# Kernel optimization log

Measured on AMD Instinct MI355X. Metric: run time of the kernel, lower is better.

Reference implementation:

```python
import jax, jax.numpy as jnp
import numpy as np

N = 50000      # nodes
E = 400000     # edges (before self loops)
IN = 128       # in_feat
HID = 64       # n_hidden per head
HEADS = [4, 4, 1]
NEG_SLOPE = 0.2  # DGL GATConv default


def gat_layer(h, src, dst, W, al, ar, b, n_nodes):
    # h: [N, Din]; W: [Din, H*F]; al/ar: [H, F]; b: [H*F]
    H, F = al.shape
    feat = (h @ W).reshape(n_nodes, H, F)              # [N,H,F]
    el = jnp.sum(feat * al, axis=-1)                   # [N,H]
    er = jnp.sum(feat * ar, axis=-1)                   # [N,H]
    e = jax.nn.leaky_relu(el[src] + er[dst], NEG_SLOPE)  # [E,H]
    # edge softmax over destination node segments (stable)
    e_max = jax.lax.stop_gradient(jax.ops.segment_max(e, dst, num_segments=n_nodes))
    ex = jnp.exp(e - e_max[dst])                       # [E,H]
    denom = jax.ops.segment_sum(ex, dst, num_segments=n_nodes)  # [N,H]
    alpha = ex / denom[dst]                            # [E,H]
    msg = feat[src] * alpha[:, :, None]                # [E,H,F]
    out = jax.ops.segment_sum(msg, dst, num_segments=n_nodes)   # [N,H,F]
    out = out + b.reshape(1, H, F)
    return out.reshape(n_nodes, H * F)


def setup_inputs() -> dict:
    key = jax.random.key(0)
    ks = jax.random.split(key, 16)
    inp = {
        "node_feat": jax.random.normal(ks[0], (N, IN), jnp.float32),
        "src": jax.random.randint(ks[1], (E,), 0, N),
        "dst": jax.random.randint(ks[2], (E,), 0, N),
    }
    dins = [IN, HID * HEADS[0], HID * HEADS[1]]
    for i, (din, h) in enumerate(zip(dins, HEADS)):
        k = 3 + 3 * i
        inp[f"W{i}"] = jax.random.normal(ks[k], (din, h * HID), jnp.float32) * 0.1
        inp[f"al{i}"] = jax.random.normal(ks[k + 1], (h, HID), jnp.float32) * 0.1
        inp[f"ar{i}"] = jax.random.normal(ks[k + 2], (h, HID), jnp.float32) * 0.1
        inp[f"b{i}"] = jnp.zeros((h * HID,), jnp.float32)
    return inp


def reference(node_feat, src, dst, W0, al0, ar0, b0, W1, al1, ar1, b1, W2, al2, ar2, b2):
    n_nodes = node_feat.shape[0]
    # add_self_loop
    loop = jnp.arange(n_nodes, dtype=src.dtype)
    src_a = jnp.concatenate([src, loop])
    dst_a = jnp.concatenate([dst, loop])
    h = node_feat
    h = gat_layer(h, src_a, dst_a, W0, al0, ar0, b0, n_nodes)  # [N, 4*64]
    h = gat_layer(h, src_a, dst_a, W1, al1, ar1, b1, n_nodes)  # [N, 4*64]
    h = gat_layer(h, src_a, dst_a, W2, al2, ar2, b2, n_nodes)  # [N, 64]
    return h
```

## Files before the change

kernel.cpp:

```cpp
#include <hip/hip_runtime.h>


typedef __attribute__((ext_vector_type(8))) short short8;
typedef __attribute__((ext_vector_type(4))) float f32x4;

__device__ __forceinline__ float bf2f(ushort u) {
  union { unsigned int i; float f; } c;
  c.i = ((unsigned int)u) << 16;
  return c.f;
}
__device__ __forceinline__ ushort f2bf(float f) {
  union { float f; unsigned int i; } c;
  c.f = f;
  unsigned int u = c.i;
  u += 0x7FFFu + ((u >> 16) & 1u);
  return (ushort)(u >> 16);
}
__device__ __forceinline__ float lrelu_exp(float x) {
  const float y = (x > 0.f) ? x : 0.2f * x;
  return __expf(y);
}

__global__ void convert_w_kernel(const float* __restrict__ W,
                                 ushort* __restrict__ Wt, int K, int N) {
  const int i = blockIdx.x * 256 + threadIdx.x;
  if (i >= K * N) return;
  const int k = i / N, n = i - k * N;
  Wt[n * K + k] = f2bf(W[i]);
}

template <bool AF32>
__global__ __launch_bounds__(256) void gemm_bf16_kernel(
    const void* __restrict__ Ap, const ushort* __restrict__ Wt,
    ushort* __restrict__ C, int M, int K, int Nc) {
  __shared__ ushort As[128][40];
  __shared__ ushort Bs[64][40];
  const int bm = blockIdx.x * 128;
  const int bn = blockIdx.y * 64;
  const int tid = threadIdx.x;
  const int lane = tid & 63;
  const int wave = tid >> 6;
  const int wm = wave >> 1;
  const int wn = wave & 1;
  const int ar = tid >> 1;
  const int ac = (tid & 1) * 16;
  const int brow = tid >> 2;
  const int bk = (tid & 3) * 8;
  const bool a_ok = (bm + ar) < M;

  f32x4 acc[4][2];
#pragma unroll
  for (int m = 0; m < 4; ++m)
#pragma unroll
    for (int n = 0; n < 2; ++n) acc[m][n] = 0.f;

  for (int k0 = 0; k0 < K; k0 += 32) {
    short8 h0, h1;
    if (AF32) {
      const float* A = (const float*)Ap;
      float buf[16];
      if (a_ok) {
        const float* p = A + (size_t)(bm + ar) * K + k0 + ac;
#pragma unroll
        for (int q = 0; q < 4; ++q) {
          float4 v = *(const float4*)(p + q * 4);
          buf[q * 4 + 0] = v.x;
          buf[q * 4 + 1] = v.y;
          buf[q * 4 + 2] = v.z;
          buf[q * 4 + 3] = v.w;
        }
      } else {
#pragma unroll
        for (int q = 0; q < 16; ++q) buf[q] = 0.f;
      }
#pragma unroll
      for (int q = 0; q < 8; ++q) h0[q] = (short)f2bf(buf[q]);
#pragma unroll
      for (int q = 0; q < 8; ++q) h1[q] = (short)f2bf(buf[8 + q]);
    } else {
      const ushort* A = (const ushort*)Ap;
      if (a_ok) {
        const ushort* p = A + (size_t)(bm + ar) * K + k0 + ac;
        h0 = *(const short8*)p;
        h1 = *(const short8*)(p + 8);
      } else {
        h0 = 0;
        h1 = 0;
      }
    }
    *(short8*)&As[ar][ac] = h0;
    *(short8*)&As[ar][ac + 8] = h1;
    *(short8*)&Bs[brow][bk] =
        *(const short8*)(Wt + (size_t)(bn + brow) * K + k0 + bk);
    __syncthreads();

    short8 a[4], b[2];
#pragma unroll
    for (int m = 0; m < 4; ++m)
      a[m] = *(const short8*)&As[wm * 64 + m * 16 + (lane & 15)][(lane >> 4) * 8];
#pragma unroll
    for (int n = 0; n < 2; ++n)
      b[n] = *(const short8*)&Bs[wn * 32 + n * 16 + (lane & 15)][(lane >> 4) * 8];
#pragma unroll
    for (int m = 0; m < 4; ++m)
#pragma unroll
      for (int n = 0; n < 2; ++n)
        acc[m][n] = __builtin_amdgcn_mfma_f32_16x16x32_bf16(a[m], b[n],
                                                            acc[m][n], 0, 0, 0);
    __syncthreads();
  }

#pragma unroll
  for (int m = 0; m < 4; ++m) {
#pragma unroll
    for (int r = 0; r < 4; ++r) {
      const int row = bm + wm * 64 + m * 16 + (lane >> 4) * 4 + r;
      if (row < M) {
#pragma unroll
        for (int n = 0; n < 2; ++n) {
          const int col = bn + wn * 32 + n * 16 + (lane & 15);
          C[(size_t)row * Nc + col] = f2bf(acc[m][n][r]);
        }
      }
    }
  }
}

__global__ __launch_bounds__(256) void attn_coef_h4(
    const ushort* __restrict__ feat, const float* __restrict__ al,
    const float* __restrict__ ar, float* __restrict__ el,
    float* __restrict__ er, int Nn) {
  const int n = (blockIdx.x * 256 + threadIdx.x) >> 6;
  const int lane = threadIdx.x & 63;
  if (n >= Nn) return;
  const short4 v = ((const short4*)(feat + (size_t)n * 256))[lane];
  const float4 a = ((const float4*)al)[lane];
  const float4 r = ((const float4*)ar)[lane];
  const float f0 = bf2f((ushort)v.x), f1 = bf2f((ushort)v.y),
              f2 = bf2f((ushort)v.z), f3 = bf2f((ushort)v.w);
  float pl = f0 * a.x + f1 * a.y + f2 * a.z + f3 * a.w;
  float pr = f0 * r.x + f1 * r.y + f2 * r.z + f3 * r.w;
#pragma unroll
  for (int off = 1; off < 16; off <<= 1) {
    pl += __shfl_xor(pl, off);
    pr += __shfl_xor(pr, off);
  }
  if ((lane & 15) == 0) {
    el[n * 4 + (lane >> 4)] = pl;
    er[n * 4 + (lane >> 4)] = pr;
  }
}

__global__ __launch_bounds__(256) void attn_coef_h1(
    const ushort* __restrict__ feat, const float* __restrict__ al,
    const float* __restrict__ ar, float* __restrict__ el,
    float* __restrict__ er, int Nn) {
  const int wid = (blockIdx.x * 256 + threadIdx.x) >> 6;
  const int lane = threadIdx.x & 63;
  const int n = wid * 4 + (lane >> 4);
  const int sub = lane & 15;
  if (n >= Nn) return;
  const short4 v = ((const short4*)(feat + (size_t)n * 64))[sub];
  const float4 a = ((const float4*)al)[sub];
  const float4 r = ((const float4*)ar)[sub];
  const float f0 = bf2f((ushort)v.x), f1 = bf2f((ushort)v.y),
              f2 = bf2f((ushort)v.z), f3 = bf2f((ushort)v.w);
  float pl = f0 * a.x + f1 * a.y + f2 * a.z + f3 * a.w;
  float pr = f0 * r.x + f1 * r.y + f2 * r.z + f3 * r.w;
#pragma unroll
  for (int off = 1; off < 16; off <<= 1) {
    pl += __shfl_xor(pl, off);
    pr += __shfl_xor(pr, off);
  }
  if (sub == 0) {
    el[n] = pl;
    er[n] = pr;
  }
}

__global__ void hist_kernel(const int* __restrict__ dst, int* __restrict__ cnt,
                            int E, int Nn) {
  const int e = blockIdx.x * blockDim.x + threadIdx.x;
  if (e >= E + Nn) return;
  const int d = (e < E) ? dst[e] : (e - E);
  atomicAdd(&cnt[d], 1);
}

__device__ __forceinline__ int block_incl_scan_1024(int x, int* lds16) {
  const int lane = threadIdx.x & 63;
  const int wid = threadIdx.x >> 6;
  int inc = x;
#pragma unroll
  for (int off = 1; off < 64; off <<= 1) {
    const int y = __shfl_up(inc, off);
    if (lane >= off) inc += y;
  }
  if (lane == 63) lds16[wid] = inc;
  __syncthreads();
  if (wid == 0) {
    int t = (lane < 16) ? lds16[lane] : 0;
#pragma unroll
    for (int off = 1; off < 16; off <<= 1) {
      const int y = __shfl_up(t, off);
      if (lane >= off) t += y;
    }
    if (lane < 16) lds16[lane] = t;
  }
  __syncthreads();
  if (wid > 0) inc += lds16[wid - 1];
  return inc;
}

__global__ __launch_bounds__(1024) void scan_blocks_kernel(
    const int* __restrict__ cnt, int* __restrict__ row_ptr,
    int* __restrict__ partials, int n) {
  __shared__ int lds16[16];
  const int i = blockIdx.x * 1024 + threadIdx.x;
  const int x = (i < n) ? cnt[i] : 0;
  const int inc = block_incl_scan_1024(x, lds16);
  if (i < n) row_ptr[i] = inc - x;
  if (threadIdx.x == 1023) partials[blockIdx.x] = inc;
}

__global__ __launch_bounds__(1024) void scan_partials_kernel(
    int* __restrict__ partials, int* __restrict__ row_ptr, int nb, int n) {
  __shared__ int lds16[16];
  const int x = (threadIdx.x < nb) ? partials[threadIdx.x] : 0;
  const int inc = block_incl_scan_1024(x, lds16);
  if (threadIdx.x < nb) partials[threadIdx.x] = inc - x;
  if (threadIdx.x == nb - 1) row_ptr[n] = inc;
}

__global__ __launch_bounds__(1024) void add_offsets_kernel(
    int* __restrict__ row_ptr, int* __restrict__ cursor,
    const int* __restrict__ partials, int n) {
  const int i = blockIdx.x * 1024 + threadIdx.x;
  if (i < n) {
    const int v = row_ptr[i] + partials[blockIdx.x];
    row_ptr[i] = v;
    cursor[i] = v;
  }
}

__global__ void scatter_kernel(const int* __restrict__ src,
                               const int* __restrict__ dst,
                               int* __restrict__ cursor, int* __restrict__ esrc,
                               int E, int Nn) {
  const int e = blockIdx.x * blockDim.x + threadIdx.x;
  if (e >= E + Nn) return;
  const int s = (e < E) ? src[e] : (e - E);
  const int d = (e < E) ? dst[e] : (e - E);
  const int pos = atomicAdd(&cursor[d], 1);
  esrc[pos] = s;
}

__global__ __launch_bounds__(256) void agg_fused_h4(
    const int* __restrict__ row_ptr, const int* __restrict__ esrc,
    const float* __restrict__ el, const float* __restrict__ er,
    const ushort* __restrict__ feat, const float* __restrict__ b,
    ushort* __restrict__ out, int Nn) {
  const int n = (blockIdx.x * 256 + threadIdx.x) >> 6;
  const int lane = threadIdx.x & 63;
  if (n >= Nn) return;
  const int h = lane >> 4;
  const int start = row_ptr[n];
  const int end = row_ptr[n + 1];
  const float erv = er[n * 4 + h];
  const short4* feat4 = (const short4*)feat;

  float den = 0.f;
  f32x4 acc = 0.f;
  int i = start;
  for (; i + 3 < end; i += 4) {
    const int s0 = esrc[i], s1 = esrc[i + 1], s2 = esrc[i + 2],
              s3 = esrc[i + 3];
    const float x0 = el[s0 * 4 + h] + erv;
    const float x1 = el[s1 * 4 + h] + erv;
    const float x2 = el[s2 * 4 + h] + erv;
    const float x3 = el[s3 * 4 + h] + erv;
    const short4 f0 = feat4[(size_t)s0 * 64 + lane];
    const short4 f1 = feat4[(size_t)s1 * 64 + lane];
    const short4 f2 = feat4[(size_t)s2 * 64 + lane];
    const short4 f3 = feat4[(size_t)s3 * 64 + lane];
    const float e0 = lrelu_exp(x0), e1 = lrelu_exp(x1), e2 = lrelu_exp(x2),
                e3 = lrelu_exp(x3);
    den += (e0 + e1) + (e2 + e3);
    acc[0] += e0 * bf2f((ushort)f0.x) + e1 * bf2f((ushort)f1.x) +
              e2 * bf2f((ushort)f2.x) + e3 * bf2f((ushort)f3.x);
    acc[1] += e0 * bf2f((ushort)f0.y) + e1 * bf2f((ushort)f1.y) +
              e2 * bf2f((ushort)f2.y) + e3 * bf2f((ushort)f3.y);
    acc[2] += e0 * bf2f((ushort)f0.z) + e1 * bf2f((ushort)f1.z) +
              e2 * bf2f((ushort)f2.z) + e3 * bf2f((ushort)f3.z);
    acc[3] += e0 * bf2f((ushort)f0.w) + e1 * bf2f((ushort)f1.w) +
              e2 * bf2f((ushort)f2.w) + e3 * bf2f((ushort)f3.w);
  }
  for (; i < end; ++i) {
    const int s = esrc[i];
    const float ex = lrelu_exp(el[s * 4 + h] + erv);
    const short4 f = feat4[(size_t)s * 64 + lane];
    den += ex;
    acc[0] += ex * bf2f((ushort)f.x);
    acc[1] += ex * bf2f((ushort)f.y);
    acc[2] += ex * bf2f((ushort)f.z);
    acc[3] += ex * bf2f((ushort)f.w);
  }
  const float rden = 1.f / den;
  const float4 bb = ((const float4*)b)[lane];
  short4 o;
  o.x = (short)f2bf(acc[0] * rden + bb.x);
  o.y = (short)f2bf(acc[1] * rden + bb.y);
  o.z = (short)f2bf(acc[2] * rden + bb.z);
  o.w = (short)f2bf(acc[3] * rden + bb.w);
  ((short4*)out)[(size_t)n * 64 + lane] = o;
}

__global__ __launch_bounds__(256) void agg_fused_h1(
    const int* __restrict__ row_ptr, const int* __restrict__ esrc,
    const float* __restrict__ el, const float* __restrict__ er,
    const ushort* __restrict__ feat, const float* __restrict__ b,
    float* __restrict__ out, int Nn) {
  const int n = (blockIdx.x * 256 + threadIdx.x) >> 6;
  const int lane = threadIdx.x & 63;
  if (n >= Nn) return;
  const int start = row_ptr[n];
  const int end = row_ptr[n + 1];
  const float erv = er[n];

  float den = 0.f;
  float acc = 0.f;
  int i = start;
  for (; i + 3 < end; i += 4) {
    const int s0 = esrc[i], s1 = esrc[i + 1], s2 = esrc[i + 2],
              s3 = esrc[i + 3];
    const float x0 = el[s0] + erv, x1 = el[s1] + erv, x2 = el[s2] + erv,
                x3 = el[s3] + erv;
    const ushort f0 = feat[(size_t)s0 * 64 + lane];
    const ushort f1 = feat[(size_t)s1 * 64 + lane];
    const ushort f2 = feat[(size_t)s2 * 64 + lane];
    const ushort f3 = feat[(size_t)s3 * 64 + lane];
    const float e0 = lrelu_exp(x0), e1 = lrelu_exp(x1), e2 = lrelu_exp(x2),
                e3 = lrelu_exp(x3);
    den += (e0 + e1) + (e2 + e3);
    acc += e0 * bf2f(f0) + e1 * bf2f(f1) + e2 * bf2f(f2) + e3 * bf2f(f3);
  }
  for (; i < end; ++i) {
    const int s = esrc[i];
    const float ex = lrelu_exp(el[s] + erv);
    den += ex;
    acc += ex * bf2f(feat[(size_t)s * 64 + lane]);
  }
  out[(size_t)n * 64 + lane] = acc * (1.f / den) + b[lane];
}

static void run_layer(const void* hin, bool af32, int K, int H, const float* W,
                      const float* al, const float* ar, const float* b,
                      ushort* Wt, ushort* feat, void* out, float* el,
                      float* er, const int* row_ptr, const int* esrc, int Nn,
                      hipStream_t stream) {
  const int HF = H * 64;
  convert_w_kernel<<<(K * HF + 255) / 256, 256, 0, stream>>>(W, Wt, K, HF);
  dim3 gg((Nn + 127) / 128, HF / 64);
  if (af32)
    gemm_bf16_kernel<true><<<gg, 256, 0, stream>>>(hin, Wt, feat, Nn, K, HF);
  else
    gemm_bf16_kernel<false><<<gg, 256, 0, stream>>>(hin, Wt, feat, Nn, K, HF);
  const int waves_grid = (Nn * 64 + 255) / 256;
  if (H == 4) {
    attn_coef_h4<<<waves_grid, 256, 0, stream>>>(feat, al, ar, el, er, Nn);
    agg_fused_h4<<<waves_grid, 256, 0, stream>>>(row_ptr, esrc, el, er, feat,
                                                 b, (ushort*)out, Nn);
  } else {
    attn_coef_h1<<<(Nn * 16 + 255) / 256, 256, 0, stream>>>(feat, al, ar, el,
                                                            er, Nn);
    agg_fused_h1<<<waves_grid, 256, 0, stream>>>(row_ptr, esrc, el, er, feat,
                                                 b, (float*)out, Nn);
  }
}

extern "C" void kernel_launch(void* const* d_in, const int* in_sizes, int n_in,
                              void* d_out, int out_size, void* d_ws,
                              size_t ws_size, hipStream_t stream) {
  const float* nf = (const float*)d_in[0];
  const int* src = (const int*)d_in[1];
  const int* dst = (const int*)d_in[2];
  const float* W0 = (const float*)d_in[3];
  const float* al0 = (const float*)d_in[4];
  const float* ar0 = (const float*)d_in[5];
  const float* b0 = (const float*)d_in[6];
  const float* W1 = (const float*)d_in[7];
  const float* al1 = (const float*)d_in[8];
  const float* ar1 = (const float*)d_in[9];
  const float* b1 = (const float*)d_in[10];
  const float* W2 = (const float*)d_in[11];
  const float* al2 = (const float*)d_in[12];
  const float* ar2 = (const float*)d_in[13];
  const float* b2 = (const float*)d_in[14];

  const int IN = 128;
  const int Nn = in_sizes[0] / IN;
  const int E = in_sizes[1];
  const int ET = E + Nn;

  char* ws = (char*)d_ws;
  size_t off = 0;
  auto alloc = [&](size_t bytes) {
    char* p = ws + off;
    off += (bytes + 255) & ~(size_t)255;
    return p;
  };
  ushort* feat = (ushort*)alloc((size_t)Nn * 256 * 2);
  ushort* h1 = (ushort*)alloc((size_t)Nn * 256 * 2);
  ushort* h2 = (ushort*)alloc((size_t)Nn * 256 * 2);
  ushort* Wt = (ushort*)alloc((size_t)256 * 256 * 2);
  float* el = (float*)alloc((size_t)Nn * 4 * 4);
  float* er = (float*)alloc((size_t)Nn * 4 * 4);
  int* row_ptr = (int*)alloc(((size_t)Nn + 1) * 4);
  int* cnt = (int*)alloc((size_t)Nn * 4);
  int* cursor = (int*)alloc((size_t)Nn * 4);
  int* esrc = (int*)alloc((size_t)ET * 4);
  int* partials = (int*)alloc((size_t)1024 * 4);
  (void)ws_size;
  (void)n_in;
  (void)out_size;

  const int nb = (Nn + 1023) / 1024;
  hipMemsetAsync(cnt, 0, (size_t)Nn * sizeof(int), stream);
  hist_kernel<<<(ET + 255) / 256, 256, 0, stream>>>(dst, cnt, E, Nn);
  scan_blocks_kernel<<<nb, 1024, 0, stream>>>(cnt, row_ptr, partials, Nn);
  scan_partials_kernel<<<1, 1024, 0, stream>>>(partials, row_ptr, nb, Nn);
  add_offsets_kernel<<<nb, 1024, 0, stream>>>(row_ptr, cursor, partials, Nn);
  scatter_kernel<<<(ET + 255) / 256, 256, 0, stream>>>(src, dst, cursor, esrc,
                                                       E, Nn);

  run_layer(nf, true, IN, 4, W0, al0, ar0, b0, Wt, feat, h1, el, er, row_ptr,
            esrc, Nn, stream);
  run_layer(h1, false, 256, 4, W1, al1, ar1, b1, Wt, feat, h2, el, er,
            row_ptr, esrc, Nn, stream);
  run_layer(h2, false, 256, 1, W2, al2, ar2, b2, Wt, feat, d_out, el, er,
            row_ptr, esrc, Nn, stream);
}
```

Before: 247.4 us.

## Pad CSR rows to multiples of four, use direct-to-LDS GEMM loads, widen tiles

Several changes land together. CSR segments are padded to multiples of 4 with a dummy node whose el is -1e9 and whose feature row is zero, so the aggregation loops drop their scalar tails. The GEMM now uses global_load_lds to copy A and W straight into LDS, and uses a 128-wide N tile for the 4-head layers. The first layer's fp32 input is converted to bf16 in a separate kernel beforehand. The single-head aggregation now handles two nodes per wave with 32-bit feature loads. These trade extra padded edges, an extra conversion pass and unpadded LDS rows, which may cause bank conflicts, for less divergence, fewer instructions and fewer GEMM blocks.

Result: faster. 235.9 us (-4.7%).

```diff
diff --git a/kernel.cpp b/kernel.cpp
--- a/kernel.cpp
+++ b/kernel.cpp
@@ -17,8 +17,28 @@
   return (ushort)(u >> 16);
 }
 __device__ __forceinline__ float lrelu_exp(float x) {
-  const float y = (x > 0.f) ? x : 0.2f * x;
+  const float y = fmaxf(x, 0.2f * x);
   return __expf(y);
+}
+__device__ __forceinline__ void gload_lds16(const ushort* g, void* lds) {
+  __builtin_amdgcn_global_load_lds(
+      (const __attribute__((address_space(1))) unsigned int*)g,
+      (__attribute__((address_space(3))) unsigned int*)lds, 16, 0, 0);
+}
+
+__global__ __launch_bounds__(256) void cvt_f32_bf16(const float* __restrict__ in,
+                                                    ushort* __restrict__ out,
+                                                    int n8) {
+  const int i = blockIdx.x * 256 + threadIdx.x;
+  if (i >= n8) return;
+  const float4 v0 = ((const float4*)in)[i * 2];
+  const float4 v1 = ((const float4*)in)[i * 2 + 1];
+  short8 o;
+  o[0] = (short)f2bf(v0.x); o[1] = (short)f2bf(v0.y);
+  o[2] = (short)f2bf(v0.z); o[3] = (short)f2bf(v0.w);
+  o[4] = (short)f2bf(v1.x); o[5] = (short)f2bf(v1.y);
+  o[6] = (short)f2bf(v1.z); o[7] = (short)f2bf(v1.w);
+  ((short8*)out)[i] = o;
 }
 
 __global__ void convert_w_kernel(const float* __restrict__ W,
@@ -29,82 +49,56 @@
   Wt[n * K + k] = f2bf(W[i]);
 }
 
-template <bool AF32>
-__global__ __launch_bounds__(256) void gemm_bf16_kernel(
-    const void* __restrict__ Ap, const ushort* __restrict__ Wt,
+template <int BN>
+__global__ __launch_bounds__(256) void gemm_mfma(
+    const ushort* __restrict__ A, const ushort* __restrict__ Wt,
     ushort* __restrict__ C, int M, int K, int Nc) {
-  __shared__ ushort As[128][40];
-  __shared__ ushort Bs[64][40];
+  constexpr int NF = BN / 32;
+  __shared__ ushort As[128][32];
+  __shared__ ushort Bs[BN][32];
   const int bm = blockIdx.x * 128;
-  const int bn = blockIdx.y * 64;
+  const int bn = blockIdx.y * BN;
   const int tid = threadIdx.x;
   const int lane = tid & 63;
   const int wave = tid >> 6;
   const int wm = wave >> 1;
   const int wn = wave & 1;
-  const int ar = tid >> 1;
-  const int ac = (tid & 1) * 16;
-  const int brow = tid >> 2;
-  const int bk = (tid & 3) * 8;
-  const bool a_ok = (bm + ar) < M;
-
-  f32x4 acc[4][2];
+
+  f32x4 acc[4][NF];
 #pragma unroll
   for (int m = 0; m < 4; ++m)
 #pragma unroll
-    for (int n = 0; n < 2; ++n) acc[m][n] = 0.f;
+    for (int n = 0; n < NF; ++n) acc[m][n] = 0.f;
 
   for (int k0 = 0; k0 < K; k0 += 32) {
-    short8 h0, h1;
-    if (AF32) {
-      const float* A = (const float*)Ap;
-      float buf[16];
-      if (a_ok) {
-        const float* p = A + (size_t)(bm + ar) * K + k0 + ac;
-#pragma unroll
-        for (int q = 0; q < 4; ++q) {
-          float4 v = *(const float4*)(p + q * 4);
-          buf[q * 4 + 0] = v.x;
-          buf[q * 4 + 1] = v.y;
-          buf[q * 4 + 2] = v.z;
-          buf[q * 4 + 3] = v.w;
-        }
-      } else {
-#pragma unroll
-        for (int q = 0; q < 16; ++q) buf[q] = 0.f;
-      }
-#pragma unroll
-      for (int q = 0; q < 8; ++q) h0[q] = (short)f2bf(buf[q]);
-#pragma unroll
-      for (int q = 0; q < 8; ++q) h1[q] = (short)f2bf(buf[8 + q]);
-    } else {
-      const ushort* A = (const ushort*)Ap;
-      if (a_ok) {
-        const ushort* p = A + (size_t)(bm + ar) * K + k0 + ac;
-        h0 = *(const short8*)p;
-        h1 = *(const short8*)(p + 8);
-      } else {
-        h0 = 0;
-        h1 = 0;
-      }
+#pragma unroll
+    for (int c = wave; c < 8; c += 4) {
+      const int row = c * 16 + (lane >> 2);
+      int rg = bm + row;
+      if (rg >= M) rg = M - 1;
+      gload_lds16(A + (size_t)rg * K + k0 + (lane & 3) * 8,
+                  (char*)(&As[0][0]) + c * 1024);
     }
-    *(short8*)&As[ar][ac] = h0;
-    *(short8*)&As[ar][ac + 8] = h1;
-    *(short8*)&Bs[brow][bk] =
-        *(const short8*)(Wt + (size_t)(bn + brow) * K + k0 + bk);
+#pragma unroll
+    for (int c = wave; c < BN / 16; c += 4) {
+      const int row = c * 16 + (lane >> 2);
+      gload_lds16(Wt + (size_t)(bn + row) * K + k0 + (lane & 3) * 8,
+                  (char*)(&Bs[0][0]) + c * 1024);
+    }
     __syncthreads();
 
-    short8 a[4], b[2];
+    short8 a[4], b[NF];
 #pragma unroll
     for (int m = 0; m < 4; ++m)
       a[m] = *(const short8*)&As[wm * 64 + m * 16 + (lane & 15)][(lane >> 4) * 8];
 #pragma unroll
-    for (int n = 0; n < 2; ++n)
-      b[n] = *(const short8*)&Bs[wn * 32 + n * 16 + (lane & 15)][(lane >> 4) * 8];
+    for (int n = 0; n < NF; ++n)
+      b[n] = *(const short8*)&Bs[wn * (NF * 16) + n * 16 + (lane & 15)]
+                             [(lane >> 4) * 8];
 #pragma unroll
     for (int m = 0; m < 4; ++m)
 #pragma unroll
-      for (int n = 0; n < 2; ++n)
+      for (int n = 0; n < NF; ++n)
         acc[m][n] = __builtin_amdgcn_mfma_f32_16x16x32_bf16(a[m], b[n],
                                                             acc[m][n], 0, 0, 0);
     __syncthreads();
@@ -117,8 +111,8 @@
       const int row = bm + wm * 64 + m * 16 + (lane >> 4) * 4 + r;
       if (row < M) {
 #pragma unroll
-        for (int n = 0; n < 2; ++n) {
-          const int col = bn + wn * 32 + n * 16 + (lane & 15);
+        for (int n = 0; n < NF; ++n) {
+          const int col = bn + wn * (NF * 16) + n * 16 + (lane & 15);
           C[(size_t)row * Nc + col] = f2bf(acc[m][n][r]);
         }
       }
@@ -130,6 +124,7 @@
     const ushort* __restrict__ feat, const float* __restrict__ al,
     const float* __restrict__ ar, float* __restrict__ el,
     float* __restrict__ er, int Nn) {
+  if (blockIdx.x == 0 && threadIdx.x < 4) el[Nn * 4 + threadIdx.x] = -1e9f;
   const int n = (blockIdx.x * 256 + threadIdx.x) >> 6;
   const int lane = threadIdx.x & 63;
   if (n >= Nn) return;
@@ -155,6 +150,7 @@
     const ushort* __restrict__ feat, const float* __restrict__ al,
     const float* __restrict__ ar, float* __restrict__ el,
     float* __restrict__ er, int Nn) {
+  if (blockIdx.x == 0 && threadIdx.x == 0) el[Nn] = -1e9f;
   const int wid = (blockIdx.x * 256 + threadIdx.x) >> 6;
   const int lane = threadIdx.x & 63;
   const int n = wid * 4 + (lane >> 4);
@@ -216,7 +212,7 @@
     int* __restrict__ partials, int n) {
   __shared__ int lds16[16];
   const int i = blockIdx.x * 1024 + threadIdx.x;
-  const int x = (i < n) ? cnt[i] : 0;
+  const int x = (i < n) ? ((cnt[i] + 3) & ~3) : 0;
   const int inc = block_incl_scan_1024(x, lds16);
   if (i < n) row_ptr[i] = inc - x;
   if (threadIdx.x == 1023) partials[blockIdx.x] = inc;
@@ -252,6 +248,15 @@
   const int d = (e < E) ? dst[e] : (e - E);
   const int pos = atomicAdd(&cursor[d], 1);
   esrc[pos] = s;
+}
+
+__global__ void fill_pad_kernel(const int* __restrict__ cursor,
+                                const int* __restrict__ row_ptr,
+                                int* __restrict__ esrc, int Nn) {
+  const int n = blockIdx.x * 256 + threadIdx.x;
+  if (n >= Nn) return;
+  const int end = row_ptr[n + 1];
+  for (int p = cursor[n]; p < end; ++p) esrc[p] = Nn;
 }
 
 __global__ __launch_bounds__(256) void agg_fused_h4(
@@ -270,20 +275,19 @@
 
   float den = 0.f;
   f32x4 acc = 0.f;
-  int i = start;
-  for (; i + 3 < end; i += 4) {
+  for (int i = start; i < end; i += 4) {
     const int s0 = esrc[i], s1 = esrc[i + 1], s2 = esrc[i + 2],
               s3 = esrc[i + 3];
-    const float x0 = el[s0 * 4 + h] + erv;
-    const float x1 = el[s1 * 4 + h] + erv;
-    const float x2 = el[s2 * 4 + h] + erv;
-    const float x3 = el[s3 * 4 + h] + erv;
+    const float x0 = el[s0 * 4 + h];
+    const float x1 = el[s1 * 4 + h];
+    const float x2 = el[s2 * 4 + h];
+    const float x3 = el[s3 * 4 + h];
     const short4 f0 = feat4[(size_t)s0 * 64 + lane];
     const short4 f1 = feat4[(size_t)s1 * 64 + lane];
     const short4 f2 = feat4[(size_t)s2 * 64 + lane];
     const short4 f3 = feat4[(size_t)s3 * 64 + lane];
-    const float e0 = lrelu_exp(x0), e1 = lrelu_exp(x1), e2 = lrelu_exp(x2),
-                e3 = lrelu_exp(x3);
+    const float e0 = lrelu_exp(x0 + erv), e1 = lrelu_exp(x1 + erv),
+                e2 = lrelu_exp(x2 + erv), e3 = lrelu_exp(x3 + erv);
     den += (e0 + e1) + (e2 + e3);
     acc[0] += e0 * bf2f((ushort)f0.x) + e1 * bf2f((ushort)f1.x) +
               e2 * bf2f((ushort)f2.x) + e3 * bf2f((ushort)f3.x);
@@ -294,16 +298,6 @@
     acc[3] += e0 * bf2f((ushort)f0.w) + e1 * bf2f((ushort)f1.w) +
               e2 * bf2f((ushort)f2.w) + e3 * bf2f((ushort)f3.w);
   }
-  for (; i < end; ++i) {
-    const int s = esrc[i];
-    const float ex = lrelu_exp(el[s * 4 + h] + erv);
-    const short4 f = feat4[(size_t)s * 64 + lane];
-    den += ex;
-    acc[0] += ex * bf2f((ushort)f.x);
-    acc[1] += ex * bf2f((ushort)f.y);
-    acc[2] += ex * bf2f((ushort)f.z);
-    acc[3] += ex * bf2f((ushort)f.w);
-  }
   const float rden = 1.f / den;
   const float4 bb = ((const float4*)b)[lane];
   short4 o;
@@ -319,61 +313,63 @@
     const float* __restrict__ el, const float* __restrict__ er,
     const ushort* __restrict__ feat, const float* __restrict__ b,
     float* __restrict__ out, int Nn) {
-  const int n = (blockIdx.x * 256 + threadIdx.x) >> 6;
+  const int wid = (blockIdx.x * 256 + threadIdx.x) >> 6;
   const int lane = threadIdx.x & 63;
+  const int n = wid * 2 + (lane >> 5);
+  const int sub = lane & 31;
   if (n >= Nn) return;
   const int start = row_ptr[n];
   const int end = row_ptr[n + 1];
   const float erv = er[n];
+  const uint* feat2 = (const uint*)feat;
 
   float den = 0.f;
-  float acc = 0.f;
-  int i = start;
-  for (; i + 3 < end; i += 4) {
+  float a0 = 0.f, a1 = 0.f;
+  for (int i = start; i < end; i += 4) {
     const int s0 = esrc[i], s1 = esrc[i + 1], s2 = esrc[i + 2],
               s3 = esrc[i + 3];
-    const float x0 = el[s0] + erv, x1 = el[s1] + erv, x2 = el[s2] + erv,
-                x3 = el[s3] + erv;
-    const ushort f0 = feat[(size_t)s0 * 64 + lane];
-    const ushort f1 = feat[(size_t)s1 * 64 + lane];
-    const ushort f2 = feat[(size_t)s2 * 64 + lane];
-    const ushort f3 = feat[(size_t)s3 * 64 + lane];
-    const float e0 = lrelu_exp(x0), e1 = lrelu_exp(x1), e2 = lrelu_exp(x2),
-                e3 = lrelu_exp(x3);
+    const float x0 = el[s0], x1 = el[s1], x2 = el[s2], x3 = el[s3];
+    const uint f0 = feat2[(size_t)s0 * 32 + sub];
+    const uint f1 = feat2[(size_t)s1 * 32 + sub];
+    const uint f2 = feat2[(size_t)s2 * 32 + sub];
+    const uint f3 = feat2[(size_t)s3 * 32 + sub];
+    const float e0 = lrelu_exp(x0 + erv), e1 = lrelu_exp(x1 + erv),
+                e2 = lrelu_exp(x2 + erv), e3 = lrelu_exp(x3 + erv);
     den += (e0 + e1) + (e2 + e3);
-    acc += e0 * bf2f(f0) + e1 * bf2f(f1) + e2 * bf2f(f2) + e3 * bf2f(f3);
-  }
-  for (; i < end; ++i) {
-    const int s = esrc[i];
-    const float ex = lrelu_exp(el[s] + erv);
-    den += ex;
-    acc += ex * bf2f(feat[(size_t)s * 64 + lane]);
-  }
-  out[(size_t)n * 64 + lane] = acc * (1.f / den) + b[lane];
-}
-
-static void run_layer(const void* hin, bool af32, int K, int H, const float* W,
+    a0 += e0 * bf2f((ushort)(f0 & 0xffff)) + e1 * bf2f((ushort)(f1 & 0xffff)) +
+          e2 * bf2f((ushort)(f2 & 0xffff)) + e3 * bf2f((ushort)(f3 & 0xffff));
+    a1 += e0 * bf2f((ushort)(f0 >> 16)) + e1 * bf2f((ushort)(f1 >> 16)) +
+          e2 * bf2f((ushort)(f2 >> 16)) + e3 * bf2f((ushort)(f3 >> 16));
+  }
+  const float rden = 1.f / den;
+  const float2 bb = ((const float2*)b)[sub];
+  float2 o;
+  o.x = a0 * rden + bb.x;
+  o.y = a1 * rden + bb.y;
+  ((float2*)out)[(size_t)n * 32 + sub] = o;
+}
+
+static void run_layer(const ushort* hin, int K, int H, const float* W,
                       const float* al, const float* ar, const float* b,
                       ushort* Wt, ushort* feat, void* out, float* el,
                       float* er, const int* row_ptr, const int* esrc, int Nn,
                       hipStream_t stream) {
   const int HF = H * 64;
   convert_w_kernel<<<(K * HF + 255) / 256, 256, 0, stream>>>(W, Wt, K, HF);
-  dim3 gg((Nn + 127) / 128, HF / 64);
-  if (af32)
-    gemm_bf16_kernel<true><<<gg, 256, 0, stream>>>(hin, Wt, feat, Nn, K, HF);
-  else
-    gemm_bf16_kernel<false><<<gg, 256, 0, stream>>>(hin, Wt, feat, Nn, K, HF);
-  const int waves_grid = (Nn * 64 + 255) / 256;
   if (H == 4) {
+    dim3 gg((Nn + 127) / 128, HF / 128);
+    gemm_mfma<128><<<gg, 256, 0, stream>>>(hin, Wt, feat, Nn, K, HF);
+    const int waves_grid = (Nn * 64 + 255) / 256;
     attn_coef_h4<<<waves_grid, 256, 0, stream>>>(feat, al, ar, el, er, Nn);
     agg_fused_h4<<<waves_grid, 256, 0, stream>>>(row_ptr, esrc, el, er, feat,
                                                  b, (ushort*)out, Nn);
   } else {
+    dim3 gg((Nn + 127) / 128, HF / 64);
+    gemm_mfma<64><<<gg, 256, 0, stream>>>(hin, Wt, feat, Nn, K, HF);
     attn_coef_h1<<<(Nn * 16 + 255) / 256, 256, 0, stream>>>(feat, al, ar, el,
                                                             er, Nn);
-    agg_fused_h1<<<waves_grid, 256, 0, stream>>>(row_ptr, esrc, el, er, feat,
-                                                 b, (float*)out, Nn);
+    agg_fused_h1<<<(Nn * 32 + 255) / 256, 256, 0, stream>>>(
+        row_ptr, esrc, el, er, feat, b, (float*)out, Nn);
   }
 }
 
@@ -399,7 +395,7 @@
   const int IN = 128;
   const int Nn = in_sizes[0] / IN;
   const int E = in_sizes[1];
-  const int ET = E + Nn;
+  const int ETP = E + 4 * Nn;
 
   char* ws = (char*)d_ws;
   size_t off = 0;
@@ -408,21 +404,27 @@
     off += (bytes + 255) & ~(size_t)255;
     return p;
   };
-  ushort* feat = (ushort*)alloc((size_t)Nn * 256 * 2);
+  ushort* feat = (ushort*)alloc(((size_t)Nn + 1) * 256 * 2);
   ushort* h1 = (ushort*)alloc((size_t)Nn * 256 * 2);
   ushort* h2 = (ushort*)alloc((size_t)Nn * 256 * 2);
+  ushort* a0 = (ushort*)alloc((size_t)Nn * 128 * 2);
   ushort* Wt = (ushort*)alloc((size_t)256 * 256 * 2);
-  float* el = (float*)alloc((size_t)Nn * 4 * 4);
+  float* el = (float*)alloc(((size_t)Nn + 1) * 4 * 4);
   float* er = (float*)alloc((size_t)Nn * 4 * 4);
   int* row_ptr = (int*)alloc(((size_t)Nn + 1) * 4);
   int* cnt = (int*)alloc((size_t)Nn * 4);
   int* cursor = (int*)alloc((size_t)Nn * 4);
-  int* esrc = (int*)alloc((size_t)ET * 4);
+  int* esrc = (int*)alloc((size_t)ETP * 4);
   int* partials = (int*)alloc((size_t)1024 * 4);
   (void)ws_size;
   (void)n_in;
   (void)out_size;
 
+  hipMemsetAsync(feat + (size_t)Nn * 256, 0, 512, stream);
+
+  cvt_f32_bf16<<<(Nn * 16 + 255) / 256, 256, 0, stream>>>(nf, a0, Nn * 16);
+
+  const int ET = E + Nn;
   const int nb = (Nn + 1023) / 1024;
   hipMemsetAsync(cnt, 0, (size_t)Nn * sizeof(int), stream);
   hist_kernel<<<(ET + 255) / 256, 256, 0, stream>>>(dst, cnt, E, Nn);
@@ -431,11 +433,13 @@
   add_offsets_kernel<<<nb, 1024, 0, stream>>>(row_ptr, cursor, partials, Nn);
   scatter_kernel<<<(ET + 255) / 256, 256, 0, stream>>>(src, dst, cursor, esrc,
                                                        E, Nn);
-
-  run_layer(nf, true, IN, 4, W0, al0, ar0, b0, Wt, feat, h1, el, er, row_ptr,
+  fill_pad_kernel<<<(Nn + 255) / 256, 256, 0, stream>>>(cursor, row_ptr, esrc,
+                                                        Nn);
+
+  run_layer(a0, IN, 4, W0, al0, ar0, b0, Wt, feat, h1, el, er, row_ptr, esrc,
+            Nn, stream);
+  run_layer(h1, 256, 4, W1, al1, ar1, b1, Wt, feat, h2, el, er, row_ptr, esrc,
+            Nn, stream);
+  run_layer(h2, 256, 1, W2, al2, ar2, b2, Wt, feat, d_out, el, er, row_ptr,
             esrc, Nn, stream);
-  run_layer(h1, false, 256, 4, W1, al1, ar1, b1, Wt, feat, h2, el, er,
-            row_ptr, esrc, Nn, stream);
-  run_layer(h2, false, 256, 1, W2, al2, ar2, b2, Wt, feat, d_out, el, er,
-            row_ptr, esrc, Nn, stream);
-}
+}
```
